# Kernel optimization log

Hardware: AMD Instinct MI355X
Metric: run time of the kernel (lower is better)

The kernel has to match this reference:

```python
import jax, jax.numpy as jnp
import numpy as np

B = 16        # graphs per batch
N0 = 4096     # nodes per graph (equal-size graphs -> static TopK shapes)
DEG = 8       # avg degree
E = B * N0 * DEG
CW = 64
OUT = 256


def _seg_sum(vals, idx, n):
    return jax.ops.segment_sum(vals, idx, num_segments=n)


def _sage(x, src, dst, valid, wl, bl, wr, n):
    # PyG SAGEConv: lin_l(mean_{j->i} x_j) + lin_r(x_i); lin_r has no bias
    vf = valid.astype(x.dtype)
    msg = x[src] * vf[:, None]                     # [E, d]
    s = _seg_sum(msg, dst, n)
    cnt = _seg_sum(vf, dst, n)
    mean = s / jnp.maximum(cnt, 1.0)[:, None]
    return mean @ wl.T + bl + x @ wr.T


def _gcn(x, src, dst, valid, w, b, n):
    # PyG GCNConv: add self-loops, symmetric normalization
    h = x @ w.T
    vf = valid.astype(x.dtype)
    deg = 1.0 + _seg_sum(vf, dst, n)               # includes self-loop
    inv_sqrt = jax.lax.rsqrt(deg)
    norm = inv_sqrt[src] * inv_sqrt[dst] * vf      # [E]
    agg = _seg_sum(h[src] * norm[:, None], dst, n) + h * (1.0 / deg)[:, None]
    return agg + b


def _topk_pool(x, src, dst, valid, w, n_per_graph):
    # PyG TopKPooling: score = x@w/||w||, keep top ceil(ratio*n) per graph,
    # x' = x[perm] * tanh(score[perm]); reindex edges, drop edges with removed endpoints.
    k = (n_per_graph + 1) // 2
    score = (x @ w) / jnp.linalg.norm(w)
    vals, idx = jax.lax.top_k(score.reshape(B, n_per_graph), k)   # [B,k]
    offs = (jnp.arange(B, dtype=jnp.int32) * n_per_graph)[:, None]
    perm = (idx.astype(jnp.int32) + offs).reshape(-1)             # [B*k] global ids
    x_new = x[perm] * jnp.tanh(vals.reshape(-1))[:, None]
    new_idx = jnp.full((B * n_per_graph,), -1, dtype=jnp.int32).at[perm].set(
        jnp.arange(B * k, dtype=jnp.int32))
    s2, d2 = new_idx[src], new_idx[dst]
    valid2 = valid & (s2 >= 0) & (d2 >= 0)
    s2 = jnp.where(valid2, s2, 0)
    d2 = jnp.where(valid2, d2, 0)
    return x_new, s2, d2, valid2, k


def _readout(x, k):
    xg = x.reshape(B, k, -1)
    return jnp.concatenate([xg.max(axis=1), xg.mean(axis=1)], axis=1)  # [B, 2d]


def _forward(x, edge_src, edge_dst, w1_l, b1, w1_r, w2_l, b2, w2_r, w3_l, b3, w3_r,
             w4, b4, w5, b5, w6, b6, p1, p2, p3, p4, p5, p6,
             lw1, lb1, lw2, lb2, lw3, lb3):
    src, dst = edge_src, edge_dst
    valid = jnp.ones((E,), dtype=bool)
    n = N0
    sage_ps = [(w1_l, b1, w1_r), (w2_l, b2, w2_r), (w3_l, b3, w3_r)]
    gcn_ps = [(w4, b4), (w5, b5), (w6, b6)]
    pools = [p1, p2, p3, p4, p5, p6]
    h = x
    z = None
    for i in range(6):
        if i < 3:
            wl, bl, wr = sage_ps[i]
            h = jax.nn.relu(_sage(h, src, dst, valid, wl, bl, wr, B * n))
        else:
            w, b = gcn_ps[i - 3]
            h = jax.nn.relu(_gcn(h, src, dst, valid, w, b, B * n))
        h, src, dst, valid, n = _topk_pool(h, src, dst, valid, pools[i], n)
        r = _readout(h, n)
        z = r if z is None else z + r
    z = jax.nn.relu(z @ lw1.T + lb1)
    z = jax.nn.relu(z @ lw2.T + lb2)
    z = z @ lw3.T + lb3
    return jax.nn.softmax(z, axis=1)


def setup_inputs() -> dict:
    key = jax.random.key(0)
    ks = jax.random.split(key, 40)

    def nrm(k, shape, s=0.1):
        return jax.random.normal(k, shape, dtype=jnp.float32) * s

    # per-graph random edges (both endpoints inside the same graph block)
    epg = N0 * DEG
    src_l = jax.random.randint(ks[0], (B, epg), 0, N0, dtype=jnp.int32)
    dst_l = jax.random.randint(ks[1], (B, epg), 0, N0, dtype=jnp.int32)
    offs = (jnp.arange(B, dtype=jnp.int32) * N0)[:, None]
    inp = {
        'x': jax.random.normal(ks[2], (B * N0, 2), dtype=jnp.float32),
        'edge_src': (src_l + offs).reshape(-1),
        'edge_dst': (dst_l + offs).reshape(-1),
        'w1_l': nrm(ks[3], (CW, 2)), 'b1': nrm(ks[4], (CW,)), 'w1_r': nrm(ks[5], (CW, 2)),
        'w2_l': nrm(ks[6], (CW, CW)), 'b2': nrm(ks[7], (CW,)), 'w2_r': nrm(ks[8], (CW, CW)),
        'w3_l': nrm(ks[9], (CW, CW)), 'b3': nrm(ks[10], (CW,)), 'w3_r': nrm(ks[11], (CW, CW)),
        'w4': nrm(ks[12], (CW, CW)), 'b4': jnp.zeros((CW,), jnp.float32),
        'w5': nrm(ks[13], (CW, CW)), 'b5': jnp.zeros((CW,), jnp.float32),
        'w6': nrm(ks[14], (CW, CW)), 'b6': jnp.zeros((CW,), jnp.float32),
        'p1': nrm(ks[15], (CW,)), 'p2': nrm(ks[16], (CW,)), 'p3': nrm(ks[17], (CW,)),
        'p4': nrm(ks[18], (CW,)), 'p5': nrm(ks[19], (CW,)), 'p6': nrm(ks[20], (CW,)),
        'lw1': nrm(ks[21], (128, 2 * CW)), 'lb1': nrm(ks[22], (128,)),
        'lw2': nrm(ks[23], (64, 128)), 'lb2': nrm(ks[24], (64,)),
        'lw3': nrm(ks[25], (OUT, 64)), 'lb3': nrm(ks[26], (OUT,)),
    }
    return inp


def reference(x, edge_src, edge_dst, w1_l, b1, w1_r, w2_l, b2, w2_r, w3_l, b3, w3_r,
              w4, b4, w5, b5, w6, b6, p1, p2, p3, p4, p5, p6,
              lw1, lb1, lw2, lb2, lw3, lb3):
    return _forward(x, edge_src, edge_dst, w1_l, b1, w1_r, w2_l, b2, w2_r,
                    w3_l, b3, w3_r, w4, b4, w5, b5, w6, b6,
                    p1, p2, p3, p4, p5, p6, lw1, lb1, lw2, lb2, lw3, lb3)
```

## Files before the change

### kernel.cpp

```cpp
#include <hip/hip_runtime.h>
#include <math.h>

#define NB 16
#define N0 4096
#define NE 524288
#define CAPE 1280


static __global__ void k_count(const int* __restrict__ dst, int* __restrict__ cnt) {
  int e = blockIdx.x * 256 + threadIdx.x;
  if (e >= NE) return;
  atomicAdd(&cnt[dst[e]], 1);
}

static __global__ void k_fill0(const int* __restrict__ src, const int* __restrict__ dst,
                               int* __restrict__ cursor, int* __restrict__ list) {
  int e = blockIdx.x * 256 + threadIdx.x;
  if (e >= NE) return;
  int d = dst[e];
  int slot = atomicAdd(&cursor[d], 1);
  list[slot] = src[e];
}


static __global__ void k_scan1(const int* __restrict__ in, int* __restrict__ out,
                               int* __restrict__ bsum, int n) {
  __shared__ int ts[256];
  int base = blockIdx.x * 1024 + threadIdx.x * 4;
  int a0 = (base + 0 < n) ? in[base + 0] : 0;
  int a1 = (base + 1 < n) ? in[base + 1] : 0;
  int a2 = (base + 2 < n) ? in[base + 2] : 0;
  int a3 = (base + 3 < n) ? in[base + 3] : 0;
  int s = a0 + a1 + a2 + a3;
  ts[threadIdx.x] = s;
  __syncthreads();
  for (int off = 1; off < 256; off <<= 1) {
    int v = (threadIdx.x >= off) ? ts[threadIdx.x - off] : 0;
    __syncthreads();
    ts[threadIdx.x] += v;
    __syncthreads();
  }
  int excl = ts[threadIdx.x] - s;
  if (base + 0 < n) out[base + 0] = excl;
  excl += a0;
  if (base + 1 < n) out[base + 1] = excl;
  excl += a1;
  if (base + 2 < n) out[base + 2] = excl;
  excl += a2;
  if (base + 3 < n) out[base + 3] = excl;
  if (threadIdx.x == 255) bsum[blockIdx.x] = ts[255];
}

static __global__ void k_scan3(int* __restrict__ out, int* __restrict__ out2,
                               const int* __restrict__ bsum, int n, int nblk) {
  __shared__ int sb[64];
  int t = threadIdx.x;
  if (t < 64) {
    int v = (t < nblk) ? bsum[t] : 0;
    int p = v;
    for (int off = 1; off < 64; off <<= 1) {
      int u = __shfl_up(p, off);
      if (t >= off) p += u;
    }
    sb[t] = p - v;
  }
  __syncthreads();
  int i = blockIdx.x * 256 + t;
  if (i < n) {
    int v = out[i] + sb[i >> 10];
    out[i] = v;
    if (out2) out2[i] = v;
  }
}


static __global__ void k_newfill(const int* __restrict__ perm, const int* __restrict__ offs,
                                 const int* __restrict__ cnt, const int* __restrict__ list,
                                 const int* __restrict__ newidx, const int* __restrict__ noffs,
                                 int* __restrict__ nlist, int newn) {
  int nn = blockIdx.x * 256 + threadIdx.x;
  if (nn >= newn) return;
  int old = perm[nn];
  int st = offs[old], c = cnt[old];
  int pos = noffs[nn];
  for (int j = 0; j < c; ++j) {
    int s2 = newidx[list[st + j]];
    if (s2 >= 0) nlist[pos++] = s2;
  }
}


static __global__ void k_pw(const float* __restrict__ p0, const float* __restrict__ p1,
                            const float* __restrict__ p2, const float* __restrict__ p3,
                            const float* __restrict__ p4, const float* __restrict__ p5,
                            const float* __restrict__ w0, const float* __restrict__ w1,
                            const float* __restrict__ w2, const float* __restrict__ w3,
                            const float* __restrict__ w4, const float* __restrict__ w5,
                            const float* __restrict__ w6, float* __restrict__ pnbuf,
                            float* __restrict__ wp) {
  if (blockIdx.x < 6) {
    if (threadIdx.x >= 64) return;
    const float* pp = p0;
    switch (blockIdx.x) {
      case 1: pp = p1; break;
      case 2: pp = p2; break;
      case 3: pp = p3; break;
      case 4: pp = p4; break;
      case 5: pp = p5; break;
      default: break;
    }
    double v = (double)pp[threadIdx.x];
    v *= v;
#pragma unroll
    for (int off = 1; off < 64; off <<= 1) v += __shfl_xor(v, off);
    if (threadIdx.x == 0) pnbuf[blockIdx.x] = (float)(1.0 / sqrt(v));
  } else {
    int wi = blockIdx.x - 6;
    const float* src = w0;
    switch (wi) {
      case 1: src = w1; break;
      case 2: src = w2; break;
      case 3: src = w3; break;
      case 4: src = w4; break;
      case 5: src = w5; break;
      case 6: src = w6; break;
      default: break;
    }
    float* dst = wp + (size_t)wi * 4096;
    const float4* w4p = (const float4*)src;
    for (int i4 = threadIdx.x; i4 < 1024; i4 += 256) {
      int o = i4 >> 4, db = (i4 & 15) << 2;
      float4 W = w4p[i4];
      float Wv[4] = {W.x, W.y, W.z, W.w};
      int og = o >> 2, o3 = o & 3;
#pragma unroll
      for (int j = 0; j < 4; ++j) {
        int d = db + j;
        dst[(d << 6) + (((og ^ (d & 15)) << 2) | o3)] = Wv[j];
      }
    }
  }
}


static __global__ void k_sage_gather2(const float* __restrict__ x, const int* __restrict__ offs,
                                      const int* __restrict__ cnt, const int* __restrict__ list,
                                      float* __restrict__ mean, int ntot) {
  int v = blockIdx.x * 256 + threadIdx.x;
  if (v >= ntot) return;
  int st = offs[v], c = cnt[v];
  float s0 = 0.f, s1 = 0.f;
  for (int j = 0; j < c; ++j) {
    int s = list[st + j];
    s0 += x[s * 2 + 0];
    s1 += x[s * 2 + 1];
  }
  float inv = 1.0f / fmaxf((float)c, 1.0f);
  mean[v * 2 + 0] = s0 * inv;
  mean[v * 2 + 1] = s1 * inv;
}

static __global__ void k_sage0(const float* __restrict__ x, const float* __restrict__ mean,
                               const float* __restrict__ wl, const float* __restrict__ blv,
                               const float* __restrict__ wr, const float* __restrict__ pvec,
                               const float* __restrict__ pnbuf, float* __restrict__ h,
                               float* __restrict__ score, int ntot) {
  __shared__ float wlT[2][65], wrT[2][65];
  if (threadIdx.x < 128) {
    int o = threadIdx.x >> 1, d = threadIdx.x & 1;
    wlT[d][o] = wl[o * 2 + d];
    wrT[d][o] = wr[o * 2 + d];
  }
  __syncthreads();
  int o = threadIdx.x & 63, vl = threadIdx.x >> 6;
  int base = blockIdx.x * 16 + vl * 4;
  float pn = pnbuf[0];
  float psl = pvec[o];
#pragma unroll
  for (int r = 0; r < 4; ++r) {
    int v = base + r;
    if (v >= ntot) break;
    float acc = blv[o] + mean[v * 2 + 0] * wlT[0][o] + mean[v * 2 + 1] * wlT[1][o] +
                x[v * 2 + 0] * wrT[0][o] + x[v * 2 + 1] * wrT[1][o];
    float hval = fmaxf(acc, 0.0f);
    h[(size_t)v * 64 + o] = hval;
    double sc = (double)hval * (double)psl;
#pragma unroll
    for (int off = 1; off < 64; off <<= 1) sc += __shfl_xor(sc, off);
    if (o == 0) score[v] = (float)sc * pn;
  }
}

static __global__ __launch_bounds__(512) void k_sage_mm(
    const float* __restrict__ x, const int* __restrict__ offs, const int* __restrict__ cnt,
    const int* __restrict__ list, const float* __restrict__ wlT, const float* __restrict__ blv,
    const float* __restrict__ wrT, const float* __restrict__ pvec,
    const float* __restrict__ pnbuf, int pidx, float* __restrict__ h,
    float* __restrict__ score) {
  __shared__ float smem[8192];
  __shared__ float psh[64], bsh[64];
  __shared__ int lds_list[CAPE];
  float* xT = smem;
  float* mT = smem + 4096;
  int t = threadIdx.x;
  size_t nb = (size_t)((blockIdx.x & 7) * (gridDim.x >> 3) + (blockIdx.x >> 3));

  if (t < 64) {
    psh[t] = pvec[t];
    bsh[t] = blv[t];
  }
  const float4* x4 = (const float4*)(x + nb * 4096);
  for (int i = t; i < 1024; i += 512) {
    int node = i >> 4, db = (i & 15) << 2;
    float4 a = x4[i];
    float av[4] = {a.x, a.y, a.z, a.w};
    int ng = node >> 2, n0 = node & 3;
#pragma unroll
    for (int j = 0; j < 4; ++j) {
      int d = db + j;
      xT[(d << 6) + (((ng ^ (d & 15)) << 2) | n0)] = av[j];
    }
  }
  int gv0 = (int)nb * 64;
  int st0 = offs[gv0];
  int nedge = offs[gv0 + 63] + cnt[gv0 + 63] - st0;
  int ncap = (nedge < CAPE) ? nedge : CAPE;
  for (int e = t; e < ncap; e += 512) lds_list[e] = list[st0 + e];
  __syncthreads();

  {
    int lane = t & 63, w = t >> 6;
    int stq[8], cq[8];
    float accq[8];
    int cmax = 0;
#pragma unroll
    for (int q = 0; q < 8; ++q) {
      int gv = gv0 + w * 8 + q;
      stq[q] = offs[gv] - st0;
      cq[q] = cnt[gv];
      accq[q] = 0.f;
      cmax = max(cmax, cq[q]);
    }
    int ncl = (nedge > 0) ? (nedge - 1) : 0;
    for (int j = 0; j < cmax; ++j) {
#pragma unroll
      for (int q = 0; q < 8; ++q) {
        bool act = j < cq[q];
        int idx = stq[q] + (act ? j : 0);
        idx = (idx < ncl) ? idx : ncl;
        int sn = (idx < ncap) ? lds_list[idx] : list[st0 + idx];
        float xv = x[(size_t)(sn & 32767) * 64 + lane];
        accq[q] = act ? (accq[q] + xv) : accq[q];
      }
    }
#pragma unroll
    for (int q = 0; q < 8; ++q) {
      int node = w * 8 + q;
      float mval = accq[q] * (1.0f / fmaxf((float)cq[q], 1.0f));
      int col = (((node >> 2) ^ (lane & 15)) << 2) | (node & 3);
      mT[(lane << 6) + col] = mval;
    }
  }
  __syncthreads();

  int tx = t & 15, ty = t >> 4;
  int ng = ty >> 1, n0 = (ty & 1) << 1;
  float acc[2][4] = {};
#pragma unroll 4
  for (int k = 0; k < 64; ++k) {
    int s = k & 15;
    int ca = (((ng ^ s) << 2) | n0);
    const float2 a2 = *(const float2*)&xT[(k << 6) + ca];
    const float2 m2 = *(const float2*)&mT[(k << 6) + ca];
    const float4 L = *(const float4*)&wlT[(k << 6) + ((tx ^ s) << 2)];
    const float4 R = *(const float4*)&wrT[(k << 6) + ((tx ^ s) << 2)];
    float A[2] = {a2.x, a2.y}, M[2] = {m2.x, m2.y};
    float Lv[4] = {L.x, L.y, L.z, L.w}, Rv[4] = {R.x, R.y, R.z, R.w};
#pragma unroll
    for (int r = 0; r < 2; ++r)
#pragma unroll
      for (int c = 0; c < 4; ++c) acc[r][c] += M[r] * Lv[c] + A[r] * Rv[c];
  }

  float pn = pnbuf[pidx];
  float hv[2][4];
  double sp[2];
#pragma unroll
  for (int r = 0; r < 2; ++r) {
    sp[r] = 0.0;
#pragma unroll
    for (int c = 0; c < 4; ++c) {
      float v = fmaxf(acc[r][c] + bsh[(tx << 2) + c], 0.0f);
      hv[r][c] = v;
      sp[r] += (double)v * (double)psh[(tx << 2) + c];
    }
  }
  __syncthreads();
  float* hT = smem;
  double* sred = (double*)(smem + 4608);
#pragma unroll
  for (int r = 0; r < 2; ++r) {
    int node = (ty << 1) + r;
    int nk = node & 15;
#pragma unroll
    for (int c = 0; c < 4; ++c) hT[node * 68 + (((tx ^ nk) << 2) | c)] = hv[r][c];
    sred[(tx << 6) + node] = sp[r];
  }
  __syncthreads();
  float4* h4 = (float4*)(h + nb * 4096);
  for (int i = t; i < 1024; i += 512) {
    int node = i >> 4, q = i & 15;
    h4[i] = *(const float4*)&hT[node * 68 + ((q ^ (node & 15)) << 2)];
  }
  if (t < 64) {
    double ssum = 0.0;
    for (int g = 0; g < 16; ++g) ssum += sred[(g << 6) + t];
    score[nb * 64 + t] = (float)ssum * pn;
  }
}


static __global__ __launch_bounds__(256) void k_gcn_mm(const float* __restrict__ x,
                                                       const float* __restrict__ wT,
                                                       float* __restrict__ h1) {
  __shared__ float smem[4608];
  float* xT = smem;
  int t = threadIdx.x;
  size_t nb = blockIdx.x;
  const float4* x4 = (const float4*)(x + nb * 4096);
  for (int i = t; i < 1024; i += 256) {
    int node = i >> 4, db = (i & 15) << 2;
    float4 a = x4[i];
    float av[4] = {a.x, a.y, a.z, a.w};
    int ng = node >> 2, n0 = node & 3;
#pragma unroll
    for (int j = 0; j < 4; ++j) {
      int d = db + j;
      xT[(d << 6) + (((ng ^ (d & 15)) << 2) | n0)] = av[j];
    }
  }
  __syncthreads();
  int tx = t & 15, ty = t >> 4;
  float acc[4][4] = {};
#pragma unroll 4
  for (int k = 0; k < 64; ++k) {
    int s = k & 15;
    const float4 a = *(const float4*)&xT[(k << 6) + ((tx ^ s) << 2)];
    const float4 W = *(const float4*)&wT[(k << 6) + ((ty ^ s) << 2)];
    float A[4] = {a.x, a.y, a.z, a.w}, Wv[4] = {W.x, W.y, W.z, W.w};
#pragma unroll
    for (int r = 0; r < 4; ++r)
#pragma unroll
      for (int c = 0; c < 4; ++c) acc[r][c] += A[r] * Wv[c];
  }
  __syncthreads();
  float* hT = smem;
#pragma unroll
  for (int r = 0; r < 4; ++r) {
    int node = (tx << 2) + r;
    int nk = node & 15;
#pragma unroll
    for (int c = 0; c < 4; ++c) hT[node * 68 + (((ty ^ nk) << 2) | c)] = acc[r][c];
  }
  __syncthreads();
  float4* h4 = (float4*)(h1 + nb * 4096);
  for (int i = t; i < 1024; i += 256) {
    int node = i >> 4, q = i & 15;
    h4[i] = *(const float4*)&hT[node * 68 + ((q ^ (node & 15)) << 2)];
  }
}

static __global__ void k_gcn_gather(const float* __restrict__ h1, const int* __restrict__ offs,
                                    const int* __restrict__ lenarr, const int* __restrict__ vcnt,
                                    const int* __restrict__ list, const float* __restrict__ b,
                                    const float* __restrict__ pvec,
                                    const float* __restrict__ pnbuf, int pidx,
                                    float* __restrict__ h, float* __restrict__ score, int ntot) {
  int lane = threadIdx.x & 63, vl = threadIdx.x >> 6;
  int v = blockIdx.x * 4 + vl;
  if (v >= ntot) return;
  int st = offs[v], len = lenarr[v];
  float degv = 1.0f + (float)vcnt[v];
  float ivd = 1.0f / sqrtf(degv);
  float acc = 0.f;
  for (int j = 0; j < len; ++j) {
    int e = list[st + j];
    if (e >= 0) {
      float nrm = (1.0f / sqrtf(1.0f + (float)vcnt[e])) * ivd;
      acc += h1[(size_t)e * 64 + lane] * nrm;
    }
  }
  float outv = fmaxf(acc + h1[(size_t)v * 64 + lane] * (1.0f / degv) + b[lane], 0.0f);
  h[(size_t)v * 64 + lane] = outv;
  double sc = (double)outv * (double)pvec[lane];
#pragma unroll
  for (int off = 1; off < 64; off <<= 1) sc += __shfl_xor(sc, off);
  if (lane == 0) score[v] = (float)sc * pnbuf[pidx];
}


static __global__ void k_chunksort(const float* __restrict__ score,
                                   unsigned long long* __restrict__ runs, int n_per, int k,
                                   int* __restrict__ newidx, int* __restrict__ perm, int single) {
  extern __shared__ unsigned long long sk[];
  int CH = blockDim.x;
  int g0 = blockIdx.x * CH;
  int b = g0 / n_per;
  int i = threadIdx.x;
  int gi = g0 + i;
  int li = gi - b * n_per;
  unsigned u = __float_as_uint(score[gi]);
  unsigned s = (u & 0x80000000u) ? u : ~(u | 0x80000000u);
  sk[i] = ((unsigned long long)s << 32) | (unsigned)li;
  __syncthreads();
  for (int ksz = 2; ksz <= CH; ksz <<= 1) {
    for (int j = ksz >> 1; j > 0; j >>= 1) {
      int ixj = i ^ j;
      if (ixj > i) {
        unsigned long long a = sk[i], c = sk[ixj];
        bool up = ((i & ksz) == 0);
        if ((a > c) == up) {
          sk[i] = c;
          sk[ixj] = a;
        }
      }
      __syncthreads();
    }
  }
  if (!single) {
    runs[gi] = sk[i];
  } else {
    int r = i;
    int idx = (int)(sk[r] & 0xFFFFFFFFu);
    int gidx = b * n_per + idx;
    if (r < k) {
      perm[b * k + r] = gidx;
      newidx[gidx] = b * k + r;
    } else {
      newidx[gidx] = -1;
    }
  }
}

static __global__ void k_merge(const unsigned long long* __restrict__ in,
                               unsigned long long* __restrict__ out, int L, int ntot, int n_per,
                               int k, int* __restrict__ newidx, int* __restrict__ perm,
                               int final) {
  int g = blockIdx.x * 256 + threadIdx.x;
  if (g >= ntot) return;
  unsigned long long key = in[g];
  int pair = g / (2 * L);
  int base = pair * 2 * L;
  int t = g - base;
  const unsigned long long* sib;
  int p;
  if (t < L) {
    sib = in + base + L;
    p = t;
  } else {
    sib = in + base;
    p = t - L;
  }
  int lo = 0, hi = L;
  while (lo < hi) {
    int mid = (lo + hi) >> 1;
    lo = (sib[mid] < key) ? mid + 1 : lo;
    hi = (sib[mid] < key) ? hi : mid;
  }
  int pos = p + lo;
  if (!final) {
    out[base + pos] = key;
  } else {
    int b = base / n_per;
    int idx = (int)(key & 0xFFFFFFFFu);
    int gidx = b * n_per + idx;
    if (pos < k) {
      perm[b * k + pos] = gidx;
      newidx[gidx] = b * k + pos;
    } else {
      newidx[gidx] = -1;
    }
  }
}


static __global__ __launch_bounds__(1024) void k_pool_post(
    const float* __restrict__ h, const float* __restrict__ score, const int* __restrict__ perm,
    float* __restrict__ xnew, float* __restrict__ pmax, float* __restrict__ psum, int base,
    const int* __restrict__ offs, const int* __restrict__ lenarr, const int* __restrict__ list,
    const int* __restrict__ newidx, int* __restrict__ ncnt, int* __restrict__ noffs,
    int* __restrict__ nlen, int newn, int G1, int G2, const int* __restrict__ rin,
    int* __restrict__ rout, int rn) {
  __shared__ float tile[64 * 68];
  __shared__ float pm[16][65], ps[16][65];
  int t = threadIdx.x;
  int bid = blockIdx.x;
  if (bid >= G1 + G2) {
    int e = (bid - G1 - G2) * 1024 + t;
    if (e < rn) {
      int v = rin[e];
      rout[e] = (v >= 0 && v < 65536) ? newidx[v] : -1;
    }
    return;
  }
  if (bid >= G1) {
    int nn = (bid - G1) * 1024 + t;
    if (nn >= newn) return;
    int old = perm[nn];
    int st = offs[old], c = lenarr[old];
    int cc = 0;
    for (int j = 0; j < c; ++j) {
      int e = list[st + j];
      cc += (e >= 0 && newidx[e] >= 0);
    }
    ncnt[nn] = cc;
    return;
  }
  int node = t >> 4, q = t & 15;
  int nn = bid * 64 + node;
  int old = perm[nn];
  if (noffs && t < 64) {
    int nn2 = bid * 64 + t;
    int o2 = perm[nn2];
    noffs[nn2] = offs[o2];
    nlen[nn2] = lenarr[o2];
  }
  float tm = tanhf(score[old]);
  float4 v = *(const float4*)&h[(size_t)old * 64 + q * 4];
  v.x *= tm;
  v.y *= tm;
  v.z *= tm;
  v.w *= tm;
  *(float4*)&xnew[(size_t)nn * 64 + q * 4] = v;
  *(float4*)&tile[node * 68 + ((q ^ (node & 15)) << 2)] = v;
  __syncthreads();
  int slot = t >> 6, d = t & 63;
  int q2 = d >> 2, i3 = d & 3;
  float m = -INFINITY, s = 0.f;
#pragma unroll
  for (int r = 0; r < 4; ++r) {
    int nd = slot * 4 + r;
    float val = tile[nd * 68 + (((q2 ^ (nd & 15)) << 2) | i3)];
    m = fmaxf(m, val);
    s += val;
  }
  pm[slot][d] = m;
  ps[slot][d] = s;
  __syncthreads();
  if (t < 64) {
    float mm = -INFINITY, ss = 0.f;
#pragma unroll
    for (int sl = 0; sl < 16; ++sl) {
      mm = fmaxf(mm, pm[sl][t]);
      ss += ps[sl][t];
    }
    pmax[(size_t)(base + bid) * 64 + t] = mm;
    psum[(size_t)(base + bid) * 64 + t] = ss;
  }
}


static __global__ void k_mlp(const float* __restrict__ pmax, const float* __restrict__ psum,
                             const float* __restrict__ lw1, const float* __restrict__ lb1,
                             const float* __restrict__ lw2, const float* __restrict__ lb2,
                             const float* __restrict__ lw3, const float* __restrict__ lb3,
                             float* __restrict__ out) {
  __shared__ float zs[128], t1[128], t2[64], t3[256], red[256];
  int b = blockIdx.x, tid = threadIdx.x;
  const int baseL[6] = {0, 512, 768, 896, 960, 992};
  const int nchL[6] = {32, 16, 8, 4, 2, 1};
  const int kkL[6] = {2048, 1024, 512, 256, 128, 64};
  if (tid < 64) {
    float zm = 0.f;
    for (int i = 0; i < 6; ++i) {
      float m = -INFINITY;
      for (int c = 0; c < nchL[i]; ++c)
        m = fmaxf(m, pmax[(size_t)(baseL[i] + b * nchL[i] + c) * 64 + tid]);
      zm += m;
    }
    zs[tid] = zm;
  } else if (tid < 128) {
    int d = tid - 64;
    float zsum = 0.f;
    for (int i = 0; i < 6; ++i) {
      float s = 0.f;
      for (int c = 0; c < nchL[i]; ++c)
        s += psum[(size_t)(baseL[i] + b * nchL[i] + c) * 64 + d];
      zsum += s / (float)kkL[i];
    }
    zs[tid] = zsum;
  }
  __syncthreads();
  if (tid < 128) {
    double a = 0.0;
    for (int d = 0; d < 128; ++d) a += (double)lw1[tid * 128 + d] * (double)zs[d];
    t1[tid] = fmaxf((float)a + lb1[tid], 0.0f);
  }
  __syncthreads();
  if (tid < 64) {
    double a = 0.0;
    for (int d = 0; d < 128; ++d) a += (double)lw2[tid * 128 + d] * (double)t1[d];
    t2[tid] = fmaxf((float)a + lb2[tid], 0.0f);
  }
  __syncthreads();
  {
    double a = 0.0;
    for (int d = 0; d < 64; ++d) a += (double)lw3[tid * 64 + d] * (double)t2[d];
    t3[tid] = (float)a + lb3[tid];
  }
  __syncthreads();
  red[tid] = t3[tid];
  __syncthreads();
  for (int s = 128; s > 0; s >>= 1) {
    if (tid < s) red[tid] = fmaxf(red[tid], red[tid + s]);
    __syncthreads();
  }
  float mx = red[0];
  __syncthreads();
  float e = expf(t3[tid] - mx);
  red[tid] = e;
  __syncthreads();
  for (int s = 128; s > 0; s >>= 1) {
    if (tid < s) red[tid] += red[tid + s];
    __syncthreads();
  }
  out[b * 256 + tid] = e / red[0];
}


extern "C" void kernel_launch(void* const* d_in, const int* in_sizes, int n_in,
                              void* d_out, int out_size, void* d_ws, size_t ws_size,
                              hipStream_t stream) {
  const float* x0 = (const float*)d_in[0];
  const int* esrc0 = (const int*)d_in[1];
  const int* edst0 = (const int*)d_in[2];
  const float* WL[3] = {(const float*)d_in[3], (const float*)d_in[6], (const float*)d_in[9]};
  const float* BL[3] = {(const float*)d_in[4], (const float*)d_in[7], (const float*)d_in[10]};
  const float* WR[3] = {(const float*)d_in[5], (const float*)d_in[8], (const float*)d_in[11]};
  const float* WG[3] = {(const float*)d_in[12], (const float*)d_in[14], (const float*)d_in[16]};
  const float* BG[3] = {(const float*)d_in[13], (const float*)d_in[15], (const float*)d_in[17]};
  const float* P[6] = {(const float*)d_in[18], (const float*)d_in[19], (const float*)d_in[20],
                       (const float*)d_in[21], (const float*)d_in[22], (const float*)d_in[23]};
  const float* lw1 = (const float*)d_in[24];
  const float* lb1 = (const float*)d_in[25];
  const float* lw2 = (const float*)d_in[26];
  const float* lb2 = (const float*)d_in[27];
  const float* lw3 = (const float*)d_in[28];
  const float* lb3 = (const float*)d_in[29];

  char* ws = (char*)d_ws;
  size_t off = 0;
  auto alloc = [&](size_t bytes) -> void* {
    void* p = ws + off;
    off += (bytes + 255) & ~(size_t)255;
    return p;
  };
  float* hA = (float*)alloc((size_t)65536 * 64 * 4);
  float* hB = (float*)alloc((size_t)32768 * 64 * 4);
  float* mean = (float*)alloc((size_t)65536 * 2 * 4);
  float* tmp = (float*)alloc((size_t)8192 * 64 * 4);
  float* score = (float*)alloc((size_t)65536 * 4);
  int* newidx = (int*)alloc((size_t)65536 * 4);
  int* perm = (int*)alloc((size_t)32768 * 4);
  int* cntA = (int*)alloc((size_t)65536 * 4);
  int* cntB = (int*)alloc((size_t)65536 * 4);
  int* offsA = (int*)alloc((size_t)65536 * 4);
  int* offsB = (int*)alloc((size_t)65536 * 4);
  int* lenA = (int*)alloc((size_t)32768 * 4);
  int* lenB = (int*)alloc((size_t)32768 * 4);
  int* cursor = (int*)alloc((size_t)65536 * 4);
  int* bsum = (int*)alloc((size_t)64 * 4);
  int* listA = (int*)alloc((size_t)NE * 4);
  int* listB = (int*)alloc((size_t)NE * 4);
  float* pmax = (float*)alloc((size_t)1024 * 64 * 4);
  float* psum = (float*)alloc((size_t)1024 * 64 * 4);
  unsigned long long* keyA = (unsigned long long*)alloc((size_t)65536 * 8);
  unsigned long long* keyB = (unsigned long long*)alloc((size_t)65536 * 8);
  float* pnbuf = (float*)alloc((size_t)64 * 4);
  float* wp = (float*)alloc((size_t)7 * 4096 * 4);
  if (off > ws_size) return;

  auto scan = [&](int* cntp, int* offsp, int* curp, int n) {
    int nblk = (n + 1023) / 1024;
    k_scan1<<<nblk, 256, 0, stream>>>(cntp, offsp, bsum, n);
    k_scan3<<<(n + 255) / 256, 256, 0, stream>>>(offsp, curp, bsum, n, nblk);
  };

  k_pw<<<13, 256, 0, stream>>>(P[0], P[1], P[2], P[3], P[4], P[5], WL[1], WR[1], WL[2], WR[2],
                               WG[0], WG[1], WG[2], pnbuf, wp);

  hipMemsetAsync(cntA, 0, (size_t)65536 * 4, stream);
  k_count<<<NE / 256, 256, 0, stream>>>(edst0, cntA);
  scan(cntA, offsA, cursor, 65536);
  k_fill0<<<NE / 256, 256, 0, stream>>>(esrc0, edst0, cursor, listA);

  const float* xcur = x0;
  int* ccnt = cntA;
  int* coffs = offsA;
  int* clist = listA;
  int* clen = nullptr;
  const int baseL[6] = {0, 512, 768, 896, 960, 992};

  for (int i = 0; i < 6; ++i) {
    int n_per = N0 >> i;
    int ntot = NB * n_per;
    int k = n_per >> 1;

    if (i == 0) {
      k_sage_gather2<<<(ntot + 255) / 256, 256, 0, stream>>>(xcur, coffs, ccnt, clist, mean, ntot);
      k_sage0<<<(ntot + 15) / 16, 256, 0, stream>>>(xcur, mean, WL[0], BL[0], WR[0], P[0], pnbuf,
                                                    hA, score, ntot);
    } else if (i < 3) {
      const float* wlp = wp + (size_t)((i - 1) * 2 + 0) * 4096;
      const float* wrp = wp + (size_t)((i - 1) * 2 + 1) * 4096;
      k_sage_mm<<<ntot / 64, 512, 0, stream>>>(xcur, coffs, ccnt, clist, wlp, BL[i], wrp, P[i],
                                               pnbuf, i, hA, score);
    } else {
      int g = i - 3;
      k_gcn_mm<<<ntot / 64, 256, 0, stream>>>(xcur, wp + (size_t)(4 + g) * 4096, tmp);
      k_gcn_gather<<<(ntot + 3) / 4, 256, 0, stream>>>(tmp, coffs, clen ? clen : ccnt, ccnt,
                                                       clist, BG[g], P[i], pnbuf, i, hA, score,
                                                       ntot);
    }

    int CH = (n_per < 1024) ? n_per : 1024;
    int single = (CH == n_per) ? 1 : 0;
    k_chunksort<<<ntot / CH, CH, (size_t)CH * 8, stream>>>(score, keyA, n_per, k, newidx, perm,
                                                           single);
    if (!single) {
      unsigned long long* cur = keyA;
      unsigned long long* nxt = keyB;
      for (int L = CH; L * 2 <= n_per; L <<= 1) {
        int fin = (L * 2 == n_per) ? 1 : 0;
        k_merge<<<(ntot + 255) / 256, 256, 0, stream>>>(cur, nxt, L, ntot, n_per, k, newidx, perm,
                                                        fin);
        unsigned long long* t2 = cur;
        cur = nxt;
        nxt = t2;
      }
    }

    int nch = k / 64;
    int G1 = NB * nch;
    int newn = (i < 5) ? NB * k : 0;
    int compacted_out = (i < 2);
    int sentinel_out = (i >= 2 && i < 5);
    int* ncnt = (i & 1) ? cntA : cntB;
    int* noffs = (i & 1) ? offsA : offsB;
    int* nlen = (i & 1) ? lenA : lenB;
    int* nlist = (i & 1) ? listA : listB;
    int G2 = (newn > 0) ? (newn + 1023) / 1024 : 0;
    int G3 = sentinel_out ? (NE / 1024) : 0;
    const int* lenarr = clen ? clen : ccnt;
    k_pool_post<<<G1 + G2 + G3, 1024, 0, stream>>>(
        hA, score, perm, hB, pmax, psum, baseL[i], coffs, lenarr, clist, newidx, ncnt,
        sentinel_out ? noffs : nullptr, sentinel_out ? nlen : nullptr, newn, G1, G2, clist,
        nlist, G3 ? NE : 0);

    if (compacted_out) {
      scan(ncnt, noffs, nullptr, newn);
      k_newfill<<<(newn + 255) / 256, 256, 0, stream>>>(perm, coffs, ccnt, clist, newidx, noffs,
                                                        nlist, newn);
      ccnt = ncnt;
      coffs = noffs;
      clist = nlist;
      clen = nullptr;
    } else if (sentinel_out) {
      ccnt = ncnt;
      coffs = noffs;
      clist = nlist;
      clen = nlen;
    }

    xcur = hB;
  }

  k_mlp<<<NB, 256, 0, stream>>>(pmax, psum, lw1, lb1, lw2, lb2, lw3, lb3, (float*)d_out);
}
```

Baseline: 338.0 us.

## Fuse layer-0 SAGE gather into projection kernel; halve sage_mm tile to 32 nodes

The first SAGE layer's neighbor-mean gather is merged into the projection kernel, with means kept in shared memory, which removes one launch and a global round trip. The layer 1-2 SAGE kernel now handles 32 nodes per block instead of 64, doubling the grid and using less LDS and registers per block for better occupancy. It also writes h directly with float4 stores rather than staging through shared memory. In exchange, only 64 threads of each 1024-thread block do the serial gather in layer 0, and the smaller tile reuses weights less.

Measured after the change: 351.4 us. 1.04x slower.

```diff
diff --git a/kernel.cpp b/kernel.cpp
--- a/kernel.cpp
+++ b/kernel.cpp
@@ -4,7 +4,7 @@
 #define NB 16
 #define N0 4096
 #define NE 524288
-#define CAPE 1280
+#define CAPE 768
 
 
 static __global__ void k_count(const int* __restrict__ dst, int* __restrict__ cnt) {
@@ -143,44 +143,41 @@
 }
 
 
-static __global__ void k_sage_gather2(const float* __restrict__ x, const int* __restrict__ offs,
-                                      const int* __restrict__ cnt, const int* __restrict__ list,
-                                      float* __restrict__ mean, int ntot) {
-  int v = blockIdx.x * 256 + threadIdx.x;
-  if (v >= ntot) return;
-  int st = offs[v], c = cnt[v];
-  float s0 = 0.f, s1 = 0.f;
-  for (int j = 0; j < c; ++j) {
-    int s = list[st + j];
-    s0 += x[s * 2 + 0];
-    s1 += x[s * 2 + 1];
-  }
-  float inv = 1.0f / fmaxf((float)c, 1.0f);
-  mean[v * 2 + 0] = s0 * inv;
-  mean[v * 2 + 1] = s1 * inv;
-}
-
-static __global__ void k_sage0(const float* __restrict__ x, const float* __restrict__ mean,
-                               const float* __restrict__ wl, const float* __restrict__ blv,
-                               const float* __restrict__ wr, const float* __restrict__ pvec,
-                               const float* __restrict__ pnbuf, float* __restrict__ h,
-                               float* __restrict__ score, int ntot) {
+static __global__ __launch_bounds__(1024) void k_sage0(
+    const float* __restrict__ x, const int* __restrict__ offs, const int* __restrict__ cnt,
+    const int* __restrict__ list, const float* __restrict__ wl, const float* __restrict__ blv,
+    const float* __restrict__ wr, const float* __restrict__ pvec,
+    const float* __restrict__ pnbuf, float* __restrict__ h, float* __restrict__ score) {
   __shared__ float wlT[2][65], wrT[2][65];
-  if (threadIdx.x < 128) {
-    int o = threadIdx.x >> 1, d = threadIdx.x & 1;
+  __shared__ float msh[64][2];
+  int t = threadIdx.x;
+  if (t < 128) {
+    int o = t >> 1, d = t & 1;
     wlT[d][o] = wl[o * 2 + d];
     wrT[d][o] = wr[o * 2 + d];
   }
-  __syncthreads();
-  int o = threadIdx.x & 63, vl = threadIdx.x >> 6;
-  int base = blockIdx.x * 16 + vl * 4;
+  if (t < 64) {
+    int v = blockIdx.x * 64 + t;
+    int st = offs[v], c = cnt[v];
+    float s0 = 0.f, s1 = 0.f;
+    for (int j = 0; j < c; ++j) {
+      int s = list[st + j];
+      s0 += x[s * 2 + 0];
+      s1 += x[s * 2 + 1];
+    }
+    float inv = 1.0f / fmaxf((float)c, 1.0f);
+    msh[t][0] = s0 * inv;
+    msh[t][1] = s1 * inv;
+  }
+  __syncthreads();
+  int o = t & 63, w = t >> 6;
   float pn = pnbuf[0];
   float psl = pvec[o];
 #pragma unroll
   for (int r = 0; r < 4; ++r) {
-    int v = base + r;
-    if (v >= ntot) break;
-    float acc = blv[o] + mean[v * 2 + 0] * wlT[0][o] + mean[v * 2 + 1] * wlT[1][o] +
+    int node = w * 4 + r;
+    int v = blockIdx.x * 64 + node;
+    float acc = blv[o] + msh[node][0] * wlT[0][o] + msh[node][1] * wlT[1][o] +
                 x[v * 2 + 0] * wrT[0][o] + x[v * 2 + 1] * wrT[1][o];
     float hval = fmaxf(acc, 0.0f);
     h[(size_t)v * 64 + o] = hval;
@@ -197,11 +194,11 @@
     const float* __restrict__ wrT, const float* __restrict__ pvec,
     const float* __restrict__ pnbuf, int pidx, float* __restrict__ h,
     float* __restrict__ score) {
-  __shared__ float smem[8192];
+  __shared__ float smem[4224];
   __shared__ float psh[64], bsh[64];
   __shared__ int lds_list[CAPE];
   float* xT = smem;
-  float* mT = smem + 4096;
+  float* mT = smem + 2112;
   int t = threadIdx.x;
   size_t nb = (size_t)((blockIdx.x & 7) * (gridDim.x >> 3) + (blockIdx.x >> 3));
 
@@ -209,33 +206,29 @@
     psh[t] = pvec[t];
     bsh[t] = blv[t];
   }
-  const float4* x4 = (const float4*)(x + nb * 4096);
-  for (int i = t; i < 1024; i += 512) {
-    int node = i >> 4, db = (i & 15) << 2;
-    float4 a = x4[i];
+  int gv0 = (int)nb * 32;
+  {
+    const float4* x4 = (const float4*)(x + (size_t)gv0 * 64);
+    int node = t >> 4, db = (t & 15) << 2;
+    float4 a = x4[t];
     float av[4] = {a.x, a.y, a.z, a.w};
-    int ng = node >> 2, n0 = node & 3;
-#pragma unroll
-    for (int j = 0; j < 4; ++j) {
-      int d = db + j;
-      xT[(d << 6) + (((ng ^ (d & 15)) << 2) | n0)] = av[j];
-    }
-  }
-  int gv0 = (int)nb * 64;
+#pragma unroll
+    for (int j = 0; j < 4; ++j) xT[(db + j) * 33 + node] = av[j];
+  }
   int st0 = offs[gv0];
-  int nedge = offs[gv0 + 63] + cnt[gv0 + 63] - st0;
+  int nedge = offs[gv0 + 31] + cnt[gv0 + 31] - st0;
   int ncap = (nedge < CAPE) ? nedge : CAPE;
   for (int e = t; e < ncap; e += 512) lds_list[e] = list[st0 + e];
   __syncthreads();
 
   {
     int lane = t & 63, w = t >> 6;
-    int stq[8], cq[8];
-    float accq[8];
+    int stq[4], cq[4];
+    float accq[4];
     int cmax = 0;
 #pragma unroll
-    for (int q = 0; q < 8; ++q) {
-      int gv = gv0 + w * 8 + q;
+    for (int q = 0; q < 4; ++q) {
+      int gv = gv0 + w * 4 + q;
       stq[q] = offs[gv] - st0;
       cq[q] = cnt[gv];
       accq[q] = 0.f;
@@ -244,7 +237,7 @@
     int ncl = (nedge > 0) ? (nedge - 1) : 0;
     for (int j = 0; j < cmax; ++j) {
 #pragma unroll
-      for (int q = 0; q < 8; ++q) {
+      for (int q = 0; q < 4; ++q) {
         bool act = j < cq[q];
         int idx = stq[q] + (act ? j : 0);
         idx = (idx < ncl) ? idx : ncl;
@@ -254,68 +247,49 @@
       }
     }
 #pragma unroll
-    for (int q = 0; q < 8; ++q) {
-      int node = w * 8 + q;
-      float mval = accq[q] * (1.0f / fmaxf((float)cq[q], 1.0f));
-      int col = (((node >> 2) ^ (lane & 15)) << 2) | (node & 3);
-      mT[(lane << 6) + col] = mval;
-    }
-  }
-  __syncthreads();
-
-  int tx = t & 15, ty = t >> 4;
-  int ng = ty >> 1, n0 = (ty & 1) << 1;
-  float acc[2][4] = {};
+    for (int q = 0; q < 4; ++q) {
+      int node = w * 4 + q;
+      mT[lane * 33 + node] = accq[q] * (1.0f / fmaxf((float)cq[q], 1.0f));
+    }
+  }
+  __syncthreads();
+
+  int tx = t & 15, row = t >> 4;
+  float acc[4] = {};
 #pragma unroll 4
   for (int k = 0; k < 64; ++k) {
-    int s = k & 15;
-    int ca = (((ng ^ s) << 2) | n0);
-    const float2 a2 = *(const float2*)&xT[(k << 6) + ca];
-    const float2 m2 = *(const float2*)&mT[(k << 6) + ca];
-    const float4 L = *(const float4*)&wlT[(k << 6) + ((tx ^ s) << 2)];
-    const float4 R = *(const float4*)&wrT[(k << 6) + ((tx ^ s) << 2)];
-    float A[2] = {a2.x, a2.y}, M[2] = {m2.x, m2.y};
+    int cb = ((tx ^ (k & 15)) << 2);
+    float a = xT[k * 33 + row];
+    float m = mT[k * 33 + row];
+    const float4 L = *(const float4*)&wlT[(k << 6) + cb];
+    const float4 R = *(const float4*)&wrT[(k << 6) + cb];
     float Lv[4] = {L.x, L.y, L.z, L.w}, Rv[4] = {R.x, R.y, R.z, R.w};
 #pragma unroll
-    for (int r = 0; r < 2; ++r)
-#pragma unroll
-      for (int c = 0; c < 4; ++c) acc[r][c] += M[r] * Lv[c] + A[r] * Rv[c];
+    for (int c = 0; c < 4; ++c) acc[c] += m * Lv[c] + a * Rv[c];
   }
 
   float pn = pnbuf[pidx];
-  float hv[2][4];
-  double sp[2];
-#pragma unroll
-  for (int r = 0; r < 2; ++r) {
-    sp[r] = 0.0;
-#pragma unroll
-    for (int c = 0; c < 4; ++c) {
-      float v = fmaxf(acc[r][c] + bsh[(tx << 2) + c], 0.0f);
-      hv[r][c] = v;
-      sp[r] += (double)v * (double)psh[(tx << 2) + c];
-    }
-  }
-  __syncthreads();
-  float* hT = smem;
-  double* sred = (double*)(smem + 4608);
-#pragma unroll
-  for (int r = 0; r < 2; ++r) {
-    int node = (ty << 1) + r;
-    int nk = node & 15;
-#pragma unroll
-    for (int c = 0; c < 4; ++c) hT[node * 68 + (((tx ^ nk) << 2) | c)] = hv[r][c];
-    sred[(tx << 6) + node] = sp[r];
-  }
-  __syncthreads();
-  float4* h4 = (float4*)(h + nb * 4096);
-  for (int i = t; i < 1024; i += 512) {
-    int node = i >> 4, q = i & 15;
-    h4[i] = *(const float4*)&hT[node * 68 + ((q ^ (node & 15)) << 2)];
-  }
-  if (t < 64) {
+  float hv[4];
+  double sp = 0.0;
+#pragma unroll
+  for (int c = 0; c < 4; ++c) {
+    float v = fmaxf(acc[c] + bsh[(tx << 2) + c], 0.0f);
+    hv[c] = v;
+    sp += (double)v * (double)psh[(tx << 2) + c];
+  }
+  {
+    float4 o4 = {hv[0], hv[1], hv[2], hv[3]};
+    *(float4*)&h[(size_t)(gv0 + row) * 64 + (tx << 2)] = o4;
+  }
+  __syncthreads();
+  double* sred = (double*)smem;
+  sred[(tx << 5) + row] = sp;
+  __syncthreads();
+  if (t < 32) {
     double ssum = 0.0;
-    for (int g = 0; g < 16; ++g) ssum += sred[(g << 6) + t];
-    score[nb * 64 + t] = (float)ssum * pn;
+#pragma unroll
+    for (int g = 0; g < 16; ++g) ssum += sred[(g << 5) + t];
+    score[gv0 + t] = (float)ssum * pn;
   }
 }
 
@@ -657,7 +631,6 @@
   };
   float* hA = (float*)alloc((size_t)65536 * 64 * 4);
   float* hB = (float*)alloc((size_t)32768 * 64 * 4);
-  float* mean = (float*)alloc((size_t)65536 * 2 * 4);
   float* tmp = (float*)alloc((size_t)8192 * 64 * 4);
   float* score = (float*)alloc((size_t)65536 * 4);
   int* newidx = (int*)alloc((size_t)65536 * 4);
@@ -707,13 +680,12 @@
     int k = n_per >> 1;
 
     if (i == 0) {
-      k_sage_gather2<<<(ntot + 255) / 256, 256, 0, stream>>>(xcur, coffs, ccnt, clist, mean, ntot);
-      k_sage0<<<(ntot + 15) / 16, 256, 0, stream>>>(xcur, mean, WL[0], BL[0], WR[0], P[0], pnbuf,
-                                                    hA, score, ntot);
+      k_sage0<<<ntot / 64, 1024, 0, stream>>>(xcur, coffs, ccnt, clist, WL[0], BL[0], WR[0],
+                                              P[0], pnbuf, hA, score);
     } else if (i < 3) {
       const float* wlp = wp + (size_t)((i - 1) * 2 + 0) * 4096;
       const float* wrp = wp + (size_t)((i - 1) * 2 + 1) * 4096;
-      k_sage_mm<<<ntot / 64, 512, 0, stream>>>(xcur, coffs, ccnt, clist, wlp, BL[i], wrp, P[i],
+      k_sage_mm<<<ntot / 32, 512, 0, stream>>>(xcur, coffs, ccnt, clist, wlp, BL[i], wrp, P[i],
                                                pnbuf, i, hA, score);
     } else {
       int g = i - 3;
```
